# Performance work log

Hardware: AMD Instinct MI355X
Metric: run time of the kernel (lower is better)

The kernel has to match this reference:

```python
import jax, jax.numpy as jnp
import numpy as np

EPS = 1e-16  # PyG softmax denominator epsilon


def segment_softmax(alpha, batch, num_segments):
    # alpha: (n,1); softmax within each bag (PyG-style: subtract segment max)
    m = jax.ops.segment_max(alpha, batch, num_segments=num_segments)
    e = jnp.exp(alpha - m[batch])
    s = jax.ops.segment_sum(e, batch, num_segments=num_segments)
    return e / (s[batch] + EPS)


def global_softmax_pooling(x, alpha, batch, num_segments):
    a = segment_softmax(alpha, batch, num_segments)
    return jax.ops.segment_sum(x * a, batch, num_segments=num_segments)  # (B,d)


def setup_inputs() -> dict:
    key = jax.random.key(0)
    k1, k2 = jax.random.split(key)
    n, d, B = 262144, 256, 512
    x = jax.random.normal(k1, (n, d), dtype=jnp.float32)
    batch = jnp.sort(jax.random.randint(k2, (n,), 0, B))
    return {"x": x, "batch": batch, "num_segments": B}


def reference(x, batch, num_segments):
    K = 3  # module default k
    alpha = jnp.zeros((x.shape[0], 1), dtype=x.dtype)
    for _ in range(K):  # small fixed iteration count
        z = global_softmax_pooling(x, alpha, batch, num_segments)  # (B,d)
        energy = jnp.sum(z * z, axis=1, keepdims=True)  # (B,1)
        z_squashed = jnp.sqrt(energy) / (1.0 + energy) * z  # (B,d)
        # alpha_i += <x_i, z_squashed[batch_i]> (vectorizes the per-bag mm loop)
        alpha = alpha + jnp.sum(x * z_squashed[batch], axis=1, keepdims=True)
    return global_softmax_pooling(x, alpha, batch, num_segments)
```

## Files before the change

### kernel.cpp

```cpp
#include <hip/hip_runtime.h>

#define D 256
#define CPS 4
#define TPB0 256
#define TPB1 512
#define PSTR (D + 1)

__device__ __forceinline__ unsigned bfbits(float f) {
    unsigned u = __float_as_uint(f);
    return (u + 0x7fffu + ((u >> 16) & 1u)) >> 16;
}
__device__ __forceinline__ float bflo(unsigned u) { return __uint_as_float(u << 16); }
__device__ __forceinline__ float bfhi(unsigned u) { return __uint_as_float(u & 0xffff0000u); }

__global__ __launch_bounds__(TPB0)
void bounds_k(const int* __restrict__ batch, int* __restrict__ seg_off, int n, int B)
{
    const int i = blockIdx.x * TPB0 + threadIdx.x;
    if (i >= n) return;
    const int b0 = batch[i];
    const int b1 = (i + 1 < n) ? batch[i + 1] : B;
    if (i == 0) for (int b = 0; b <= b0; ++b) seg_off[b] = 0;
    for (int b = b0 + 1; b <= b1; ++b) seg_off[b] = i + 1;
}

template<int USE_WS>
__global__ __launch_bounds__(TPB0, 8)
void pass0_k(const float* __restrict__ x, unsigned short* __restrict__ xb,
             const int* __restrict__ seg_off, float* __restrict__ part_out)
{
    __shared__ float zp[8][D];
    __shared__ float sp[8];
    const int tid = threadIdx.x;
    const int s = blockIdx.x / CPS, k = blockIdx.x % CPS;
    const int hw = tid >> 5, l = tid & 31;
    const int start = seg_off[s];
    const int cnt   = seg_off[s + 1] - start;
    const int csz   = (cnt + CPS - 1) / CPS;
    const int rbeg  = k * csz;
    const int rend  = min(cnt, rbeg + csz);

    float za[8] = {0,0,0,0,0,0,0,0};
    float s_acc = 0.f;
#pragma unroll 2
    for (int r = rbeg + hw; r < rend; r += 8) {
        const size_t boff = (size_t)(start + r) * D + l * 8;
        const float4 v0 = *(const float4*)(x + boff);
        const float4 v1 = *(const float4*)(x + boff + 4);
        if (USE_WS) {
            uint4 p;
            p.x = bfbits(v0.x) | (bfbits(v0.y) << 16);
            p.y = bfbits(v0.z) | (bfbits(v0.w) << 16);
            p.z = bfbits(v1.x) | (bfbits(v1.y) << 16);
            p.w = bfbits(v1.z) | (bfbits(v1.w) << 16);
            *(uint4*)(xb + boff) = p;
        }
        s_acc += 1.f;
        za[0] += v0.x; za[1] += v0.y; za[2] += v0.z; za[3] += v0.w;
        za[4] += v1.x; za[5] += v1.y; za[6] += v1.z; za[7] += v1.w;
    }
#pragma unroll
    for (int j = 0; j < 8; ++j) zp[hw][l * 8 + j] = za[j];
    if (l == 0) sp[hw] = s_acc;
    __syncthreads();
    float acc = 0.f;
#pragma unroll
    for (int h = 0; h < 8; ++h) acc += zp[h][tid];
    float* po = part_out + (size_t)(s * CPS + k) * PSTR;
    po[tid] = acc;
    if (tid == 0) {
        float st = 0.f;
#pragma unroll
        for (int h = 0; h < 8; ++h) st += sp[h];
        po[D] = st;
    }
}

template<int USE_WS>
__global__ __launch_bounds__(TPB1, 4)
void phases_k(const float* __restrict__ x, const unsigned short* __restrict__ xb,
              const int* __restrict__ seg_off,
              const float* __restrict__ part, float* __restrict__ out)
{
    __shared__ float zp[16][D];
    __shared__ float sp[16];
    __shared__ float zs[D];
    __shared__ float red[16];
    const int tid  = threadIdx.x;
    const int s    = blockIdx.x;
    const int slot = tid >> 5;
    const int l    = tid & 31;
    const int wv   = tid >> 6;
    const int start = seg_off[s];
    const int cnt   = seg_off[s + 1] - start;

    const float* pb = part + (size_t)s * CPS * PSTR;
    float z = 0.f;
    if (tid < D) {
#pragma unroll
        for (int kk = 0; kk < CPS; ++kk) z += pb[kk * PSTR + tid];
    }
    if (tid == 0) {
        float st = 0.f;
#pragma unroll
        for (int kk = 0; kk < CPS; ++kk) st += pb[kk * PSTR + D];
        red[0] = 1.f / (st + 1e-16f);
    }
    __syncthreads();
    z *= red[0];

    float Scol = 0.f;
    float zr[8];

    for (int ph = 1; ph <= 3; ++ph) {
        float e = (tid < D) ? z * z : 0.f;
#pragma unroll
        for (int o = 32; o; o >>= 1) e += __shfl_xor(e, o);
        if ((tid & 63) == 0) red[8 + wv] = e;
        __syncthreads();
        if (tid == 0) {
            float E = 0.f;
#pragma unroll
            for (int h = 0; h < 8; ++h) E += red[8 + h];
            red[1] = (E > 0.f) ? (sqrtf(E) / (1.f + E)) : 0.f;
        }
        __syncthreads();
        if (tid < D) { Scol += z * red[1]; zs[tid] = Scol; }
        __syncthreads();
#pragma unroll
        for (int j = 0; j < 8; ++j) zr[j] = zs[l * 8 + j];

        float za[8] = {0,0,0,0,0,0,0,0};
        float s_acc = 0.f;
        int r = slot;
        uint4 ucur = make_uint4(0,0,0,0);
        float4 c0 = {0,0,0,0}, c1 = {0,0,0,0};
        if (r < cnt) {
            const size_t o = (size_t)(start + r) * D + l * 8;
            if (USE_WS) ucur = *(const uint4*)(xb + o);
            else { c0 = *(const float4*)(x + o); c1 = *(const float4*)(x + o + 4); }
        }
        while (r < cnt) {
            const int rn = r + 16;
            uint4 unxt = make_uint4(0,0,0,0);
            float4 n0 = {0,0,0,0}, n1 = {0,0,0,0};
            if (rn < cnt) {
                const size_t o = (size_t)(start + rn) * D + l * 8;
                if (USE_WS) unxt = *(const uint4*)(xb + o);
                else { n0 = *(const float4*)(x + o); n1 = *(const float4*)(x + o + 4); }
            }
            float xf[8];
            if (USE_WS) {
                xf[0]=bflo(ucur.x); xf[1]=bfhi(ucur.x); xf[2]=bflo(ucur.y); xf[3]=bfhi(ucur.y);
                xf[4]=bflo(ucur.z); xf[5]=bfhi(ucur.z); xf[6]=bflo(ucur.w); xf[7]=bfhi(ucur.w);
            } else {
                xf[0]=c0.x; xf[1]=c0.y; xf[2]=c0.z; xf[3]=c0.w;
                xf[4]=c1.x; xf[5]=c1.y; xf[6]=c1.z; xf[7]=c1.w;
            }
            float dt = 0.f;
#pragma unroll
            for (int j = 0; j < 8; ++j) dt += xf[j] * zr[j];
#pragma unroll
            for (int o = 16; o; o >>= 1) dt += __shfl_xor(dt, o);
            const float w = __expf(dt);
            s_acc += w;
#pragma unroll
            for (int j = 0; j < 8; ++j) za[j] += w * xf[j];
            ucur = unxt; c0 = n0; c1 = n1; r = rn;
        }

#pragma unroll
        for (int j = 0; j < 8; ++j) zp[slot][l * 8 + j] = za[j];
        if (l == 0) sp[slot] = s_acc;
        __syncthreads();
        z = 0.f;
        if (tid < D) {
#pragma unroll
            for (int h = 0; h < 16; ++h) z += zp[h][tid];
        }
        if (tid == 0) {
            float st = 0.f;
#pragma unroll
            for (int h = 0; h < 16; ++h) st += sp[h];
            red[0] = 1.f / (st + 1e-16f);
        }
        __syncthreads();
        z *= red[0];
    }

    if (tid < D) out[(size_t)s * D + tid] = z;
}

extern "C" void kernel_launch(void* const* d_in, const int* in_sizes, int n_in,
                              void* d_out, int out_size, void* d_ws, size_t ws_size,
                              hipStream_t stream) {
    const float* x   = (const float*)d_in[0];
    const int* batch = (const int*)d_in[1];
    float* out       = (float*)d_out;
    const int n = in_sizes[1];
    const int B = out_size / D;

    const size_t xb_bytes = (size_t)n * D * sizeof(unsigned short);
    const size_t pe = (size_t)B * CPS * PSTR;
    const size_t small_bytes = pe * sizeof(float) + (B + 1) * sizeof(int);
    const bool use_ws = ws_size >= xb_bytes + small_bytes;

    unsigned short* xb = (unsigned short*)d_ws;
    float* pA = use_ws ? (float*)((char*)d_ws + xb_bytes) : (float*)d_ws;
    int* seg_off = (int*)(pA + pe);

    const int zgrid = (n + TPB0 - 1) / TPB0;

    bounds_k<<<zgrid, TPB0, 0, stream>>>(batch, seg_off, n, B);
    if (use_ws) {
        pass0_k<1><<<B * CPS, TPB0, 0, stream>>>(x, xb, seg_off, pA);
        phases_k<1><<<B, TPB1, 0, stream>>>(x, xb, seg_off, pA, out);
    } else {
        pass0_k<0><<<B * CPS, TPB0, 0, stream>>>(x, xb, seg_off, pA);
        phases_k<0><<<B, TPB1, 0, stream>>>(x, xb, seg_off, pA, out);
    }
}
```

Baseline: 159.2 us.

## Replace bounds kernel with in-kernel binary search and double phase-kernel block size

Removes the separate segment-bounds kernel. Each block now finds its segment start and end by binary search over the sorted batch array, which saves one launch and the seg_off round trip. The phase kernel also grows from 512 to 1024 threads per block with 32 row slots, so each segment is streamed by more warps at once. In exchange, every block pays a short serial binary search, and the larger blocks use more registers and shared memory, which may limit occupancy.

```diff
diff --git a/kernel.cpp b/kernel.cpp
--- a/kernel.cpp
+++ b/kernel.cpp
@@ -3,7 +3,8 @@
 #define D 256
 #define CPS 4
 #define TPB0 256
-#define TPB1 512
+#define TPB1 1024
+#define SLOTS 32
 #define PSTR (D + 1)
 
 __device__ __forceinline__ unsigned bfbits(float f) {
@@ -13,29 +14,27 @@
 __device__ __forceinline__ float bflo(unsigned u) { return __uint_as_float(u << 16); }
 __device__ __forceinline__ float bfhi(unsigned u) { return __uint_as_float(u & 0xffff0000u); }
 
-__global__ __launch_bounds__(TPB0)
-void bounds_k(const int* __restrict__ batch, int* __restrict__ seg_off, int n, int B)
-{
-    const int i = blockIdx.x * TPB0 + threadIdx.x;
-    if (i >= n) return;
-    const int b0 = batch[i];
-    const int b1 = (i + 1 < n) ? batch[i + 1] : B;
-    if (i == 0) for (int b = 0; b <= b0; ++b) seg_off[b] = 0;
-    for (int b = b0 + 1; b <= b1; ++b) seg_off[b] = i + 1;
-}
-
 template<int USE_WS>
 __global__ __launch_bounds__(TPB0, 8)
 void pass0_k(const float* __restrict__ x, unsigned short* __restrict__ xb,
-             const int* __restrict__ seg_off, float* __restrict__ part_out)
+             const int* __restrict__ batch, float* __restrict__ part_out, int n)
 {
     __shared__ float zp[8][D];
     __shared__ float sp[8];
+    __shared__ int bnd[2];
     const int tid = threadIdx.x;
     const int s = blockIdx.x / CPS, k = blockIdx.x % CPS;
     const int hw = tid >> 5, l = tid & 31;
-    const int start = seg_off[s];
-    const int cnt   = seg_off[s + 1] - start;
+
+    if (tid < 2) {
+        const int key = s + tid;
+        int lo = 0, hi = n;
+        while (lo < hi) { int mid = (lo + hi) >> 1; if (batch[mid] < key) lo = mid + 1; else hi = mid; }
+        bnd[tid] = lo;
+    }
+    __syncthreads();
+    const int start = bnd[0];
+    const int cnt   = bnd[1] - start;
     const int csz   = (cnt + CPS - 1) / CPS;
     const int rbeg  = k * csz;
     const int rend  = min(cnt, rbeg + csz);
@@ -77,22 +76,32 @@
 }
 
 template<int USE_WS>
-__global__ __launch_bounds__(TPB1, 4)
+__global__ __launch_bounds__(TPB1, 8)
 void phases_k(const float* __restrict__ x, const unsigned short* __restrict__ xb,
-              const int* __restrict__ seg_off,
-              const float* __restrict__ part, float* __restrict__ out)
+              const int* __restrict__ batch,
+              const float* __restrict__ part, float* __restrict__ out, int n)
 {
-    __shared__ float zp[16][D];
-    __shared__ float sp[16];
+    __shared__ float zp[SLOTS][D];
+    __shared__ float sp[SLOTS];
     __shared__ float zs[D];
-    __shared__ float red[16];
+    __shared__ float red_e[16];
+    __shared__ float red[2];
+    __shared__ int bnd[2];
     const int tid  = threadIdx.x;
     const int s    = blockIdx.x;
     const int slot = tid >> 5;
     const int l    = tid & 31;
     const int wv   = tid >> 6;
-    const int start = seg_off[s];
-    const int cnt   = seg_off[s + 1] - start;
+
+    if (tid < 2) {
+        const int key = s + tid;
+        int lo = 0, hi = n;
+        while (lo < hi) { int mid = (lo + hi) >> 1; if (batch[mid] < key) lo = mid + 1; else hi = mid; }
+        bnd[tid] = lo;
+    }
+    __syncthreads();
+    const int start = bnd[0];
+    const int cnt   = bnd[1] - start;
 
     const float* pb = part + (size_t)s * CPS * PSTR;
     float z = 0.f;
@@ -116,12 +125,12 @@
         float e = (tid < D) ? z * z : 0.f;
 #pragma unroll
         for (int o = 32; o; o >>= 1) e += __shfl_xor(e, o);
-        if ((tid & 63) == 0) red[8 + wv] = e;
+        if ((tid & 63) == 0) red_e[wv] = e;
         __syncthreads();
         if (tid == 0) {
             float E = 0.f;
 #pragma unroll
-            for (int h = 0; h < 8; ++h) E += red[8 + h];
+            for (int h = 0; h < 16; ++h) E += red_e[h];
             red[1] = (E > 0.f) ? (sqrtf(E) / (1.f + E)) : 0.f;
         }
         __syncthreads();
@@ -141,7 +150,7 @@
             else { c0 = *(const float4*)(x + o); c1 = *(const float4*)(x + o + 4); }
         }
         while (r < cnt) {
-            const int rn = r + 16;
+            const int rn = r + SLOTS;
             uint4 unxt = make_uint4(0,0,0,0);
             float4 n0 = {0,0,0,0}, n1 = {0,0,0,0};
             if (rn < cnt) {
@@ -176,12 +185,12 @@
         z = 0.f;
         if (tid < D) {
 #pragma unroll
-            for (int h = 0; h < 16; ++h) z += zp[h][tid];
+            for (int h = 0; h < SLOTS; ++h) z += zp[h][tid];
         }
         if (tid == 0) {
             float st = 0.f;
 #pragma unroll
-            for (int h = 0; h < 16; ++h) st += sp[h];
+            for (int h = 0; h < SLOTS; ++h) st += sp[h];
             red[0] = 1.f / (st + 1e-16f);
         }
         __syncthreads();
@@ -202,21 +211,16 @@
 
     const size_t xb_bytes = (size_t)n * D * sizeof(unsigned short);
     const size_t pe = (size_t)B * CPS * PSTR;
-    const size_t small_bytes = pe * sizeof(float) + (B + 1) * sizeof(int);
-    const bool use_ws = ws_size >= xb_bytes + small_bytes;
+    const bool use_ws = ws_size >= xb_bytes + pe * sizeof(float);
 
     unsigned short* xb = (unsigned short*)d_ws;
     float* pA = use_ws ? (float*)((char*)d_ws + xb_bytes) : (float*)d_ws;
-    int* seg_off = (int*)(pA + pe);
-
-    const int zgrid = (n + TPB0 - 1) / TPB0;
-
-    bounds_k<<<zgrid, TPB0, 0, stream>>>(batch, seg_off, n, B);
+
     if (use_ws) {
-        pass0_k<1><<<B * CPS, TPB0, 0, stream>>>(x, xb, seg_off, pA);
-        phases_k<1><<<B, TPB1, 0, stream>>>(x, xb, seg_off, pA, out);
+        pass0_k<1><<<B * CPS, TPB0, 0, stream>>>(x, xb, batch, pA, n);
+        phases_k<1><<<B, TPB1, 0, stream>>>(x, xb, batch, pA, out, n);
     } else {
-        pass0_k<0><<<B * CPS, TPB0, 0, stream>>>(x, xb, seg_off, pA);
-        phases_k<0><<<B, TPB1, 0, stream>>>(x, xb, seg_off, pA, out);
-    }
-}
+        pass0_k<0><<<B * CPS, TPB0, 0, stream>>>(x, xb, batch, pA, n);
+        phases_k<0><<<B, TPB1, 0, stream>>>(x, xb, batch, pA, out, n);
+    }
+}
```

Result: faster. 143.2 us, median of 2 (-10.1%).
